# Kernel tuning notes

Hardware: AMD Instinct MI355X
Metric: run time of the kernel (lower is better)

The kernel has to match this reference:

```python
import jax, jax.numpy as jnp
import numpy as np

H = 2048
W = 2048
N = H * W
NUM_CC = 1 << 20
N_ITERS = 20  # pointer-doubling covers tree depth up to 2**20 (actual depth ~ e*ln N ~ 45)
EPS = 1e-10


def _log_scaling(f):
    # f: [NUM_CC, 15] = xmin, ymin, xmax, ymax, area, angle, pca_big, pca_small, hu1..hu7
    # -> [NUM_CC, 17] = xmin..ymax, log(area), signed-log(pca_big, pca_small, hu1..hu7), lshape, cos(angle), sin(angle)
    lshape = jnp.sqrt(f[:, 7:8]) / (jnp.sqrt(f[:, 6:7]) + EPS)
    cosangle = jnp.cos(f[:, 5:6])
    sinangle = jnp.sin(f[:, 5:6])
    log_area = jnp.log(f[:, 4:5])
    signed_log = jnp.log(jnp.abs(f[:, 6:]) + EPS) * jnp.sign(f[:, 6:])
    return jnp.concatenate([f[:, :4], log_area, signed_log, lshape, cosangle, sinangle], axis=1)


def _tree_path_sum(contrib, parent):
    # out[p] = sum of contrib over p and all its ancestors (root has parent == -1).
    # Parallel pointer-doubling: after k steps acc[i] sums contrib over 2**k chain nodes.
    acc, par = contrib, parent
    for _ in range(N_ITERS):
        valid = par >= 0
        pidx = jnp.where(valid, par, 0)
        acc = acc + jnp.where(valid, acc[pidx], jnp.zeros((), acc.dtype))
        par = jnp.where(valid, par[pidx], -1)
    return acc


def setup_inputs() -> dict:
    rng = np.random.default_rng(0)
    # random recursive tree: parent[i] uniform in [0, i), root = node 0
    parent = (rng.random(N) * np.arange(N)).astype(np.int32)
    parent[0] = -1
    cc_id = rng.integers(0, NUM_CC, size=N).astype(np.int32)
    diff = rng.standard_normal(N).astype(np.float32)
    attrs = np.empty((NUM_CC, 15), np.float32)
    attrs[:, :4] = rng.random((NUM_CC, 4)) * 100.0          # bbox coords
    attrs[:, 4] = rng.random(NUM_CC) * 1000.0 + 1.0         # area (>0 for log)
    attrs[:, 5] = rng.standard_normal(NUM_CC)               # angle
    attrs[:, 6:8] = rng.random((NUM_CC, 2)) + 0.01          # pca_big/pca_small (>=0 for sqrt)
    attrs[:, 8:] = rng.standard_normal((NUM_CC, 7)).astype(np.float32)  # hu moments
    weight = ((rng.random((17, 1)) - 0.5) * 0.02).astype(np.float32)
    bias = np.zeros((1,), np.float32)
    return {
        "diff": jnp.asarray(diff),
        "attributes": jnp.asarray(attrs),
        "weight": jnp.asarray(weight),
        "bias": jnp.asarray(bias),
        "parent": jnp.asarray(parent),
        "cc_id": jnp.asarray(cc_id),
    }


def reference(diff, attributes, weight, bias, parent, cc_id):
    rescaled = _log_scaling(attributes)                                   # [NUM_CC, 17]
    cc_scores = jax.nn.sigmoid(rescaled @ weight + bias[None, :])[:, 0]   # [NUM_CC]
    contrib = diff * cc_scores[cc_id]                                     # [N]
    out = _tree_path_sum(contrib, parent)                                 # [N]
    return out.reshape(H, W)
```

## Files before the change

kernel.cpp:

```cpp
#include <hip/hip_runtime.h>
#include <hip/hip_fp16.h>

#define EPSF 1e-10f

struct alignas(8) Node { int par; float c; };

typedef int      v4i  __attribute__((ext_vector_type(4)));
typedef float    v4f  __attribute__((ext_vector_type(4)));
typedef _Float16 h4   __attribute__((ext_vector_type(4)));

__device__ __forceinline__ float signed_log(float x) {
    float sg = (x > 0.f) ? 1.f : ((x < 0.f) ? -1.f : 0.f);
    return logf(fabsf(x) + EPSF) * sg;
}

__global__ void scores_kernel(const float* __restrict__ attrs,
                              const float* __restrict__ weight,
                              const float* __restrict__ bias,
                              _Float16* __restrict__ scores, int num_cc) {
    int i = blockIdx.x * blockDim.x + threadIdx.x;
    if (i >= num_cc) return;
    const float* f = attrs + (long long)i * 15;
    float w[17];
#pragma unroll
    for (int k = 0; k < 17; ++k) w[k] = weight[k];
    float acc = bias[0];
    acc += w[0] * f[0] + w[1] * f[1] + w[2] * f[2] + w[3] * f[3];
    acc += w[4] * logf(f[4]);
#pragma unroll
    for (int j = 0; j < 9; ++j) acc += w[5 + j] * signed_log(f[6 + j]);
    float lshape = sqrtf(f[7]) / (sqrtf(f[6]) + EPSF);
    acc += w[14] * lshape;
    acc += w[15] * cosf(f[5]);
    acc += w[16] * sinf(f[5]);
    float sc = 1.f / (1.f + expf(-acc));
    __builtin_nontemporal_store((_Float16)sc, &scores[i]);
}

__global__ void pack_kernel4(const v4f* __restrict__ diff4,
                             const v4i* __restrict__ parent4,
                             const v4i* __restrict__ cc4,
                             const _Float16* __restrict__ scores,
                             v4i* __restrict__ packed2, int n4) {
    int i = blockIdx.x * blockDim.x + threadIdx.x;
    if (i >= n4) return;
    v4f d = __builtin_nontemporal_load(&diff4[i]);
    v4i p = __builtin_nontemporal_load(&parent4[i]);
    v4i c = __builtin_nontemporal_load(&cc4[i]);
    float s0 = (float)scores[c.x], s1 = (float)scores[c.y];
    float s2 = (float)scores[c.z], s3 = (float)scores[c.w];
    v4i o0, o1;
    o0.x = p.x; o0.y = __float_as_int(d.x * s0);
    o0.z = p.y; o0.w = __float_as_int(d.y * s1);
    o1.x = p.z; o1.y = __float_as_int(d.z * s2);
    o1.z = p.w; o1.w = __float_as_int(d.w * s3);
    __builtin_nontemporal_store(o0, &packed2[2 * i]);
    __builtin_nontemporal_store(o1, &packed2[2 * i + 1]);
}

__global__ void pack_kernel(const float* __restrict__ diff,
                            const int* __restrict__ parent,
                            const int* __restrict__ cc_id,
                            const _Float16* __restrict__ scores,
                            Node* __restrict__ packed, int lo, int n) {
    int i = lo + blockIdx.x * blockDim.x + threadIdx.x;
    if (i >= n) return;
    Node nd;
    nd.par = parent[i];
    nd.c = diff[i] * (float)scores[cc_id[i]];
    packed[i] = nd;
}


template <bool SH>
__global__ void walk_base(const Node* __restrict__ packed,
                          float* __restrict__ out,
                          _Float16* __restrict__ shadow, int range_end) {
    int i = blockIdx.x * blockDim.x + threadIdx.x;
    if (i >= range_end) return;
    long long raw = __builtin_nontemporal_load((const long long*)(packed + i));
    int cur = (int)(raw & 0xffffffffLL);
    float s = __int_as_float((int)(raw >> 32));
    while (cur >= 0) {
        Node nd = packed[cur];
        s += nd.c;
        cur = nd.par;
    }
    __builtin_nontemporal_store(s, &out[i]);
    if (SH) __builtin_nontemporal_store((_Float16)s, &shadow[i]);
}

template <int PX, bool SH>
__global__ void walk_phaseN(const Node* __restrict__ packed,
                            float* __restrict__ out,
                            _Float16* __restrict__ shadow, int lo, int hi) {
    long long t = (long long)blockIdx.x * blockDim.x + threadIdx.x;
    int base = lo + (int)(t * PX);
    if (base >= hi) return;
    int cur[PX]; float s[PX];

    const bool full = (base + PX <= hi);
    if (full) {
#pragma unroll
        for (int k = 0; k < PX; k += 2) {
            v4i raw = __builtin_nontemporal_load((const v4i*)(packed + base + k));
            cur[k]     = raw.x; s[k]     = __int_as_float(raw.y);
            cur[k + 1] = raw.z; s[k + 1] = __int_as_float(raw.w);
        }
    } else {
#pragma unroll
        for (int k = 0; k < PX; ++k) {
            if (base + k < hi) { Node nd = packed[base + k]; cur[k] = nd.par; s[k] = nd.c; }
            else               { cur[k] = 0; s[k] = 0.f; }
        }
    }

    while (true) {
        bool any = false;
#pragma unroll
        for (int k = 0; k < PX; ++k) any |= (cur[k] >= lo);
        if (!__any(any)) break;
#pragma unroll
        for (int k = 0; k < PX; ++k) {
            bool act = cur[k] >= lo;
            int idx = act ? cur[k] : lo;
            Node nd = packed[idx];
            s[k]  += act ? nd.c : 0.f;
            cur[k] = act ? nd.par : cur[k];
        }
    }

#pragma unroll
    for (int k = 0; k < PX; ++k)
        s[k] += SH ? (float)shadow[cur[k]] : out[cur[k]];

    if (full) {
#pragma unroll
        for (int k = 0; k < PX; k += 4) {
            v4f o; o.x = s[k]; o.y = s[k + 1]; o.z = s[k + 2]; o.w = s[k + 3];
            __builtin_nontemporal_store(o, (v4f*)(out + base + k));
            if (SH) {
                h4 hv; hv.x = (_Float16)s[k]; hv.y = (_Float16)s[k + 1];
                hv.z = (_Float16)s[k + 2];    hv.w = (_Float16)s[k + 3];
                __builtin_nontemporal_store(hv, (h4*)(shadow + base + k));
            }
        }
    } else {
#pragma unroll
        for (int k = 0; k < PX; ++k)
            if (base + k < hi) {
                out[base + k] = s[k];
                if (SH) shadow[base + k] = (_Float16)s[k];
            }
    }
}

__global__ void walk_base2(const int* __restrict__ parent,
                           const float* __restrict__ contrib,
                           float* __restrict__ out, int range_end) {
    int i = blockIdx.x * blockDim.x + threadIdx.x;
    if (i >= range_end) return;
    float s = 0.f;
    int cur = i;
    while (cur >= 0) { s += contrib[cur]; cur = parent[cur]; }
    out[i] = s;
}

__global__ void walk_phase2(const int* __restrict__ parent,
                            const float* __restrict__ contrib,
                            float* __restrict__ out, int lo, int hi) {
    int i = lo + blockIdx.x * blockDim.x + threadIdx.x;
    if (i >= hi) return;
    float s = 0.f;
    int cur = i;
    while (cur >= lo) { s += contrib[cur]; cur = parent[cur]; }
    s += out[cur];
    out[i] = s;
}

__global__ void contrib_kernel(const float* __restrict__ diff,
                               const int* __restrict__ cc_id,
                               const _Float16* __restrict__ scores,
                               float* __restrict__ contrib, int n) {
    int i = blockIdx.x * blockDim.x + threadIdx.x;
    if (i >= n) return;
    contrib[i] = diff[i] * (float)scores[cc_id[i]];
}

static inline int iminh(int a, int b) { return a < b ? a : b; }

extern "C" void kernel_launch(void* const* d_in, const int* in_sizes, int n_in,
                              void* d_out, int out_size, void* d_ws, size_t ws_size,
                              hipStream_t stream) {
    const float* diff   = (const float*)d_in[0];
    const float* attrs  = (const float*)d_in[1];
    const float* weight = (const float*)d_in[2];
    const float* bias   = (const float*)d_in[3];
    const int*   parent = (const int*)d_in[4];
    const int*   cc_id  = (const int*)d_in[5];
    float* out = (float*)d_out;

    const int n      = in_sizes[0];
    const int num_cc = in_sizes[1] / 15;

    _Float16* scores = (_Float16*)d_ws;
    const size_t scores_bytes = ((size_t)num_cc * sizeof(_Float16) + 255) & ~(size_t)255;
    const size_t packed_bytes = (size_t)n * sizeof(Node);
    const size_t shadow_bytes = (size_t)n * sizeof(_Float16);
    const bool use_packed = ws_size >= scores_bytes + packed_bytes;
    const bool use_shadow = ws_size >= scores_bytes + packed_bytes + shadow_bytes;

    const int TB = 256;
    scores_kernel<<<(num_cc + TB - 1) / TB, TB, 0, stream>>>(attrs, weight, bias, scores, num_cc);

    const int BASE = 131072;

    if (use_packed) {
        Node* packed = (Node*)((char*)d_ws + scores_bytes);
        _Float16* shadow = use_shadow ? (_Float16*)((char*)d_ws + scores_bytes + packed_bytes)
                                      : (_Float16*)nullptr;
        if ((n & 3) == 0) {
            pack_kernel4<<<(n / 4 + TB - 1) / TB, TB, 0, stream>>>(
                (const v4f*)diff, (const v4i*)parent, (const v4i*)cc_id, scores, (v4i*)packed, n / 4);
        } else {
            pack_kernel<<<(n + TB - 1) / TB, TB, 0, stream>>>(diff, parent, cc_id, scores, packed, 0, n);
        }
        int base_end = iminh(BASE, n);
        if (use_shadow)
            walk_base<true><<<(base_end + TB - 1) / TB, TB, 0, stream>>>(packed, out, shadow, base_end);
        else
            walk_base<false><<<(base_end + TB - 1) / TB, TB, 0, stream>>>(packed, out, shadow, base_end);
        int lo = base_end;
        while (lo < n) {
            long long hi_ll = (long long)lo * 2;
            int hi = (hi_ll > n) ? n : (int)hi_ll;
            int cnt = hi - lo;
            long long threads = (cnt + 3) / 4;
            int grid = (int)((threads + TB - 1) / TB);
            if (use_shadow)
                walk_phaseN<4, true><<<grid, TB, 0, stream>>>(packed, out, shadow, lo, hi);
            else
                walk_phaseN<4, false><<<grid, TB, 0, stream>>>(packed, out, shadow, lo, hi);
            lo = hi;
        }
    } else {
        float* contrib = (float*)((char*)d_ws + scores_bytes);
        contrib_kernel<<<(n + TB - 1) / TB, TB, 0, stream>>>(diff, cc_id, scores, contrib, n);
        int base_end = iminh(BASE, n);
        walk_base2<<<(base_end + TB - 1) / TB, TB, 0, stream>>>(parent, contrib, out, base_end);
        int lo = base_end;
        while (lo < n) {
            long long hi_ll = (long long)lo * 2;
            int hi = (hi_ll > n) ? n : (int)hi_ll;
            walk_phase2<<<((hi - lo) + TB - 1) / TB, TB, 0, stream>>>(parent, contrib, out, lo, hi);
            lo = hi;
        }
    }
}
```

Baseline: 124.6 us.

## Fuse packing of the next level range into each pointer-walk phase kernel

The standalone pack pass over all N nodes is replaced. Only the prologue range [0, 2*BASE) is now packed up front. Each doubling-phase walk kernel also packs the node range of the following phase, [hi, 2*hi), loading diff/parent/cc_id before the walk and storing the packed nodes after it. The aim is to hide the streaming bandwidth of packing under the latency-bound pointer-chasing loops and to save one kernel launch. In exchange, each walk thread holds more registers, which may lower occupancy. The packed path now also requires n to be a multiple of 8.

```diff
diff --git a/kernel.cpp b/kernel.cpp
--- a/kernel.cpp
+++ b/kernel.cpp
@@ -58,20 +58,6 @@
     __builtin_nontemporal_store(o1, &packed2[2 * i + 1]);
 }
 
-__global__ void pack_kernel(const float* __restrict__ diff,
-                            const int* __restrict__ parent,
-                            const int* __restrict__ cc_id,
-                            const _Float16* __restrict__ scores,
-                            Node* __restrict__ packed, int lo, int n) {
-    int i = lo + blockIdx.x * blockDim.x + threadIdx.x;
-    if (i >= n) return;
-    Node nd;
-    nd.par = parent[i];
-    nd.c = diff[i] * (float)scores[cc_id[i]];
-    packed[i] = nd;
-}
-
-
 template <bool SH>
 __global__ void walk_base(const Node* __restrict__ packed,
                           float* __restrict__ out,
@@ -91,15 +77,47 @@
 }
 
 template <int PX, bool SH>
-__global__ void walk_phaseN(const Node* __restrict__ packed,
-                            float* __restrict__ out,
-                            _Float16* __restrict__ shadow, int lo, int hi) {
+__global__ void walk_phase_fused(const Node* __restrict__ packed,
+                                 Node* __restrict__ packed_wr,
+                                 float* __restrict__ out,
+                                 _Float16* __restrict__ shadow,
+                                 const v4f* __restrict__ diff4,
+                                 const v4i* __restrict__ parent4,
+                                 const v4i* __restrict__ cc4,
+                                 const _Float16* __restrict__ scores,
+                                 int lo, int hi, int plo, int phi) {
     long long t = (long long)blockIdx.x * blockDim.x + threadIdx.x;
     int base = lo + (int)(t * PX);
-    if (base >= hi) return;
+
+    bool packv = false;
+    int pbase = phi;
+    v4f d0, d1; v4i pp0, pp1, cc0, cc1;
+    if (phi > plo) {
+        pbase = plo + (int)(t * 8);
+        if (pbase + 8 <= phi) {
+            int j = pbase >> 2;
+            d0  = __builtin_nontemporal_load(&diff4[j]);
+            d1  = __builtin_nontemporal_load(&diff4[j + 1]);
+            pp0 = __builtin_nontemporal_load(&parent4[j]);
+            pp1 = __builtin_nontemporal_load(&parent4[j + 1]);
+            cc0 = __builtin_nontemporal_load(&cc4[j]);
+            cc1 = __builtin_nontemporal_load(&cc4[j + 1]);
+            packv = true;
+        } else if (pbase < phi) {
+            const float* df = (const float*)diff4;
+            const int*   pr = (const int*)parent4;
+            const int*   cc = (const int*)cc4;
+            for (int k = 0; k < 8 && pbase + k < phi; ++k) {
+                Node nd; nd.par = pr[pbase + k];
+                nd.c = df[pbase + k] * (float)scores[cc[pbase + k]];
+                packed_wr[pbase + k] = nd;
+            }
+        }
+    }
+
     int cur[PX]; float s[PX];
-
-    const bool full = (base + PX <= hi);
+    const bool walk = (base < hi);
+    const bool full = walk && (base + PX <= hi);
     if (full) {
 #pragma unroll
         for (int k = 0; k < PX; k += 2) {
@@ -110,9 +128,17 @@
     } else {
 #pragma unroll
         for (int k = 0; k < PX; ++k) {
-            if (base + k < hi) { Node nd = packed[base + k]; cur[k] = nd.par; s[k] = nd.c; }
-            else               { cur[k] = 0; s[k] = 0.f; }
-        }
+            if (walk && base + k < hi) { Node nd = packed[base + k]; cur[k] = nd.par; s[k] = nd.c; }
+            else                       { cur[k] = lo - 1; s[k] = 0.f; }
+        }
+    }
+
+    float ps[8];
+    if (packv) {
+        ps[0] = (float)scores[cc0.x]; ps[1] = (float)scores[cc0.y];
+        ps[2] = (float)scores[cc0.z]; ps[3] = (float)scores[cc0.w];
+        ps[4] = (float)scores[cc1.x]; ps[5] = (float)scores[cc1.y];
+        ps[6] = (float)scores[cc1.z]; ps[7] = (float)scores[cc1.w];
     }
 
     while (true) {
@@ -129,6 +155,25 @@
             cur[k] = act ? nd.par : cur[k];
         }
     }
+
+    if (packv) {
+        v4i o0, o1, o2, o3;
+        o0.x = pp0.x; o0.y = __float_as_int(d0.x * ps[0]);
+        o0.z = pp0.y; o0.w = __float_as_int(d0.y * ps[1]);
+        o1.x = pp0.z; o1.y = __float_as_int(d0.z * ps[2]);
+        o1.z = pp0.w; o1.w = __float_as_int(d0.w * ps[3]);
+        o2.x = pp1.x; o2.y = __float_as_int(d1.x * ps[4]);
+        o2.z = pp1.y; o2.w = __float_as_int(d1.y * ps[5]);
+        o3.x = pp1.z; o3.y = __float_as_int(d1.z * ps[6]);
+        o3.z = pp1.w; o3.w = __float_as_int(d1.w * ps[7]);
+        v4i* dst = (v4i*)(packed_wr + pbase);
+        __builtin_nontemporal_store(o0, dst);
+        __builtin_nontemporal_store(o1, dst + 1);
+        __builtin_nontemporal_store(o2, dst + 2);
+        __builtin_nontemporal_store(o3, dst + 3);
+    }
+
+    if (!walk) return;
 
 #pragma unroll
     for (int k = 0; k < PX; ++k)
@@ -215,17 +260,14 @@
 
     const int BASE = 131072;
 
-    if (use_packed) {
+    if (use_packed && (n & 7) == 0) {
         Node* packed = (Node*)((char*)d_ws + scores_bytes);
         _Float16* shadow = use_shadow ? (_Float16*)((char*)d_ws + scores_bytes + packed_bytes)
                                       : (_Float16*)nullptr;
-        if ((n & 3) == 0) {
-            pack_kernel4<<<(n / 4 + TB - 1) / TB, TB, 0, stream>>>(
-                (const v4f*)diff, (const v4i*)parent, (const v4i*)cc_id, scores, (v4i*)packed, n / 4);
-        } else {
-            pack_kernel<<<(n + TB - 1) / TB, TB, 0, stream>>>(diff, parent, cc_id, scores, packed, 0, n);
-        }
         int base_end = iminh(BASE, n);
+        int pro_end = iminh(2 * base_end, n);
+        pack_kernel4<<<(pro_end / 4 + TB - 1) / TB, TB, 0, stream>>>(
+            (const v4f*)diff, (const v4i*)parent, (const v4i*)cc_id, scores, (v4i*)packed, pro_end / 4);
         if (use_shadow)
             walk_base<true><<<(base_end + TB - 1) / TB, TB, 0, stream>>>(packed, out, shadow, base_end);
         else
@@ -234,13 +276,23 @@
         while (lo < n) {
             long long hi_ll = (long long)lo * 2;
             int hi = (hi_ll > n) ? n : (int)hi_ll;
+            int plo = hi;
+            long long phi_ll = (long long)hi * 2;
+            int phi = (phi_ll > n) ? n : (int)phi_ll;
+            if (phi <= pro_end) phi = plo;
             int cnt = hi - lo;
             long long threads = (cnt + 3) / 4;
             int grid = (int)((threads + TB - 1) / TB);
             if (use_shadow)
-                walk_phaseN<4, true><<<grid, TB, 0, stream>>>(packed, out, shadow, lo, hi);
+                walk_phase_fused<4, true><<<grid, TB, 0, stream>>>(
+                    packed, packed, out, shadow,
+                    (const v4f*)diff, (const v4i*)parent, (const v4i*)cc_id, scores,
+                    lo, hi, plo, phi);
             else
-                walk_phaseN<4, false><<<grid, TB, 0, stream>>>(packed, out, shadow, lo, hi);
+                walk_phase_fused<4, false><<<grid, TB, 0, stream>>>(
+                    packed, packed, out, shadow,
+                    (const v4f*)diff, (const v4i*)parent, (const v4i*)cc_id, scores,
+                    lo, hi, plo, phi);
             lo = hi;
         }
     } else {
```

New measurement: 127.5 us. 1.02x slower.
